# Kernel optimization log

Hardware: AMD Instinct MI355X
Metric: run time of the kernel (lower is better)

Reference implementation:

```python
import jax, jax.numpy as jnp
import numpy as np

N_NODES = 100000
N_EDGES = 1200000
D_IN = 64
D_HID = 64
D_OUT = 64


def setup_inputs() -> dict:
    key = jax.random.key(0)
    ks = jax.random.split(key, 9)
    x = jax.random.normal(ks[0], (N_NODES, D_IN), dtype=jnp.float32)
    edge_index = jax.random.randint(ks[1], (2, N_EDGES), 0, N_NODES, dtype=jnp.int32)
    edge_attr = jax.random.uniform(ks[2], (N_EDGES,), dtype=jnp.float32)
    def lin(k, fan_in, fan_out):
        s = 1.0 / np.sqrt(fan_in)
        return jax.random.uniform(k, (fan_in, fan_out), jnp.float32, -s, s)
    W1 = lin(ks[3], D_IN, D_HID)
    b1 = jnp.zeros((D_HID,), jnp.float32)
    W2 = lin(ks[4], D_HID, D_HID)
    b2 = jnp.zeros((D_HID,), jnp.float32)
    W3 = lin(ks[5], D_HID, D_OUT)
    b3 = jnp.zeros((D_OUT,), jnp.float32)
    return {"x": x, "edge_index": edge_index, "edge_attr": edge_attr,
            "W1": W1, "b1": b1, "W2": W2, "b2": b2, "W3": W3, "b3": b3}


def _gcn_norm(edge_index, edge_weight, num_nodes):
    # PyG GCNConv default: add self-loops (weight 1) then symmetric normalization
    src, dst = edge_index[0], edge_index[1]
    loop = jnp.arange(num_nodes, dtype=src.dtype)
    src_f = jnp.concatenate([src, loop])
    dst_f = jnp.concatenate([dst, loop])
    w_f = jnp.concatenate([edge_weight, jnp.ones((num_nodes,), edge_weight.dtype)])
    deg = jax.ops.segment_sum(w_f, dst_f, num_segments=num_nodes)
    dinv = jnp.where(deg > 0, jax.lax.rsqrt(jnp.maximum(deg, 1e-30)), 0.0)
    norm = dinv[src_f] * w_f * dinv[dst_f]  # [E + N]
    return src_f, dst_f, norm


def _gcn_layer(x, src, dst, norm, W, b, num_nodes):
    h = x @ W                                   # [N, d_out] (tiny GEMM)
    msg = h[src] * norm[:, None]                # gather + scale, [E+N, d_out]
    agg = jax.ops.segment_sum(msg, dst, num_segments=num_nodes)  # scatter-add
    return agg + b


def reference(x, edge_index, edge_attr, W1, b1, W2, b2, W3, b3):
    n = x.shape[0]
    src, dst, norm = _gcn_norm(edge_index, edge_attr, n)
    h = jax.nn.relu(_gcn_layer(x, src, dst, norm, W1, b1, n))
    h = jax.nn.relu(_gcn_layer(h, src, dst, norm, W2, b2, n))
    h = jax.nn.relu(_gcn_layer(h, src, dst, norm, W3, b3, n))
    return h
```

## Files before the change

### kernel.cpp

```cpp
#include <hip/hip_runtime.h>
#include <hip/hip_bf16.h>
#include <math.h>


#define MASK44 ((1ull << 44) - 1)

__global__ __launch_bounds__(256) void init_k(unsigned long long* packed, int N) {
    int i = blockIdx.x * blockDim.x + threadIdx.x;
    if (i < N) packed[i] = 0ull;
}

__global__ __launch_bounds__(256) void edge_pass_k(const int* __restrict__ dst,
                                                   const float* __restrict__ w,
                                                   unsigned long long* __restrict__ packed,
                                                   int* __restrict__ rank, int E) {
    int t = blockIdx.x * blockDim.x + threadIdx.x;
    int e = t * 8;
    if (e + 7 < E) {
        int4   da = *(const int4*)(dst + e);
        int4   db = *(const int4*)(dst + e + 4);
        float4 wa = *(const float4*)(w + e);
        float4 wb = *(const float4*)(w + e + 4);
        unsigned long long o0 = atomicAdd(&packed[da.x], (1ull << 44) + (unsigned long long)((double)wa.x * 4294967296.0));
        unsigned long long o1 = atomicAdd(&packed[da.y], (1ull << 44) + (unsigned long long)((double)wa.y * 4294967296.0));
        unsigned long long o2 = atomicAdd(&packed[da.z], (1ull << 44) + (unsigned long long)((double)wa.z * 4294967296.0));
        unsigned long long o3 = atomicAdd(&packed[da.w], (1ull << 44) + (unsigned long long)((double)wa.w * 4294967296.0));
        unsigned long long o4 = atomicAdd(&packed[db.x], (1ull << 44) + (unsigned long long)((double)wb.x * 4294967296.0));
        unsigned long long o5 = atomicAdd(&packed[db.y], (1ull << 44) + (unsigned long long)((double)wb.y * 4294967296.0));
        unsigned long long o6 = atomicAdd(&packed[db.z], (1ull << 44) + (unsigned long long)((double)wb.z * 4294967296.0));
        unsigned long long o7 = atomicAdd(&packed[db.w], (1ull << 44) + (unsigned long long)((double)wb.w * 4294967296.0));
        *(int4*)(rank + e)     = make_int4((int)(o0 >> 44), (int)(o1 >> 44),
                                           (int)(o2 >> 44), (int)(o3 >> 44));
        *(int4*)(rank + e + 4) = make_int4((int)(o4 >> 44), (int)(o5 >> 44),
                                           (int)(o6 >> 44), (int)(o7 >> 44));
    } else {
        for (int k = e; k < E; ++k) {
            unsigned long long o =
                atomicAdd(&packed[dst[k]], (1ull << 44) + (unsigned long long)((double)w[k] * 4294967296.0));
            rank[k] = (int)(o >> 44);
        }
    }
}

__global__ __launch_bounds__(1024) void scan_block_k(const unsigned long long* __restrict__ packed,
                                                     float* __restrict__ dinv,
                                                     int* __restrict__ tmp,
                                                     int* __restrict__ bsum, int N) {
    __shared__ int sm[1024];
    int tid = threadIdx.x;
    int g = blockIdx.x * 1024 + tid;
    unsigned long long pk = (g < N) ? packed[g] : 0ull;
    int v = (int)(pk >> 44);
    if (g < N) {
        double deg = 1.0 + (double)(pk & MASK44) * (1.0 / 4294967296.0);
        dinv[g] = (float)(1.0 / sqrt(deg));
    }
    sm[tid] = v;
    __syncthreads();
    for (int off = 1; off < 1024; off <<= 1) {
        int t = (tid >= off) ? sm[tid - off] : 0;
        __syncthreads();
        sm[tid] += t;
        __syncthreads();
    }
    if (g < N) tmp[g] = sm[tid] - v;
    if (tid == 1023) bsum[blockIdx.x] = sm[1023];
}

__global__ __launch_bounds__(1024) void scan_bsums_k(int* bsum, int nb, int* rowptr, int N) {
    __shared__ int sm[1024];
    int tid = threadIdx.x;
    int v = (tid < nb) ? bsum[tid] : 0;
    sm[tid] = v;
    __syncthreads();
    for (int off = 1; off < 1024; off <<= 1) {
        int t = (tid >= off) ? sm[tid - off] : 0;
        __syncthreads();
        sm[tid] += t;
        __syncthreads();
    }
    if (tid < nb) bsum[tid] = sm[tid] - v;
    if (tid == 1023) rowptr[N] = sm[1023];
}

__global__ __launch_bounds__(1024) void scan_add_k(const int* __restrict__ tmp,
                                                   const int* __restrict__ bsum,
                                                   int* __restrict__ rowptr, int N) {
    int g = blockIdx.x * 1024 + threadIdx.x;
    if (g < N) rowptr[g] = tmp[g] + bsum[blockIdx.x];
}

__global__ __launch_bounds__(256) void fill_csr_k(const int* __restrict__ src,
                                                  const int* __restrict__ dst,
                                                  const float* __restrict__ w,
                                                  const float* __restrict__ dinv,
                                                  const int* __restrict__ rowptr,
                                                  const int* __restrict__ rank,
                                                  int2* __restrict__ csr, int E) {
    int t = blockIdx.x * blockDim.x + threadIdx.x;
    int e = t * 8;
    if (e + 7 < E) {
        int4   sa = *(const int4*)(src + e);
        int4   sb = *(const int4*)(src + e + 4);
        int4   da = *(const int4*)(dst + e);
        int4   db = *(const int4*)(dst + e + 4);
        int4   ra = *(const int4*)(rank + e);
        int4   rb = *(const int4*)(rank + e + 4);
        float4 wa = *(const float4*)(w + e);
        float4 wb = *(const float4*)(w + e + 4);
        int p0 = rowptr[da.x] + ra.x;
        int p1 = rowptr[da.y] + ra.y;
        int p2 = rowptr[da.z] + ra.z;
        int p3 = rowptr[da.w] + ra.w;
        int p4 = rowptr[db.x] + rb.x;
        int p5 = rowptr[db.y] + rb.y;
        int p6 = rowptr[db.z] + rb.z;
        int p7 = rowptr[db.w] + rb.w;
        csr[p0] = make_int2(sa.x, __float_as_int(dinv[sa.x] * wa.x * dinv[da.x]));
        csr[p1] = make_int2(sa.y, __float_as_int(dinv[sa.y] * wa.y * dinv[da.y]));
        csr[p2] = make_int2(sa.z, __float_as_int(dinv[sa.z] * wa.z * dinv[da.z]));
        csr[p3] = make_int2(sa.w, __float_as_int(dinv[sa.w] * wa.w * dinv[da.w]));
        csr[p4] = make_int2(sb.x, __float_as_int(dinv[sb.x] * wb.x * dinv[db.x]));
        csr[p5] = make_int2(sb.y, __float_as_int(dinv[sb.y] * wb.y * dinv[db.y]));
        csr[p6] = make_int2(sb.z, __float_as_int(dinv[sb.z] * wb.z * dinv[db.z]));
        csr[p7] = make_int2(sb.w, __float_as_int(dinv[sb.w] * wb.w * dinv[db.w]));
    } else {
        for (int k = e; k < E; ++k) {
            int d = dst[k], s = src[k];
            int pos = rowptr[d] + rank[k];
            csr[pos] = make_int2(s, __float_as_int(dinv[s] * w[k] * dinv[d]));
        }
    }
}

__global__ __launch_bounds__(256) void gemm64_k(const float* __restrict__ X,
                                                const float* __restrict__ W,
                                                float* __restrict__ H, int N) {
    __shared__ float Wl[64 * 64];
    __shared__ float Xl[64 * 68];
    int tid = threadIdx.x;
    for (int i = tid; i < 4096; i += 256) Wl[i] = W[i];
    int row0 = blockIdx.x * 64;
    {
        int r = tid >> 6, c = tid & 63;
        #pragma unroll
        for (int p = 0; p < 16; ++p) {
            int rr = r + 4 * p;
            int grow = row0 + rr;
            Xl[rr * 68 + c] = (grow < N) ? X[(size_t)grow * 64 + c] : 0.0f;
        }
    }
    __syncthreads();
    int tc = tid & 15, tr = tid >> 4;
    float acc[4][4];
    #pragma unroll
    for (int i = 0; i < 4; ++i)
        #pragma unroll
        for (int j = 0; j < 4; ++j) acc[i][j] = 0.0f;

    #pragma unroll 8
    for (int k = 0; k < 64; ++k) {
        float4 wv = *(const float4*)&Wl[k * 64 + 4 * tc];
        float x0 = Xl[(4 * tr + 0) * 68 + k];
        float x1 = Xl[(4 * tr + 1) * 68 + k];
        float x2 = Xl[(4 * tr + 2) * 68 + k];
        float x3 = Xl[(4 * tr + 3) * 68 + k];
        acc[0][0] += x0 * wv.x; acc[0][1] += x0 * wv.y; acc[0][2] += x0 * wv.z; acc[0][3] += x0 * wv.w;
        acc[1][0] += x1 * wv.x; acc[1][1] += x1 * wv.y; acc[1][2] += x1 * wv.z; acc[1][3] += x1 * wv.w;
        acc[2][0] += x2 * wv.x; acc[2][1] += x2 * wv.y; acc[2][2] += x2 * wv.z; acc[2][3] += x2 * wv.w;
        acc[3][0] += x3 * wv.x; acc[3][1] += x3 * wv.y; acc[3][2] += x3 * wv.z; acc[3][3] += x3 * wv.w;
    }
    #pragma unroll
    for (int i = 0; i < 4; ++i) {
        int grow = row0 + 4 * tr + i;
        if (grow < N) {
            float4 st = make_float4(acc[i][0], acc[i][1], acc[i][2], acc[i][3]);
            *(float4*)&H[(size_t)grow * 64 + 4 * tc] = st;
        }
    }
}

__global__ __launch_bounds__(256) void agg_k(const float* __restrict__ H,
                                             const int* __restrict__ rowptr,
                                             const int2* __restrict__ csr,
                                             const float* __restrict__ dinv,
                                             const float* __restrict__ bias,
                                             float* __restrict__ out, int N) {
    int wave = (blockIdx.x * blockDim.x + threadIdx.x) >> 6;
    int lane = threadIdx.x & 63;
    if (wave >= N) return;
    int i = wave;
    int g = lane >> 4;
    int l = lane & 15;

    float di = dinv[i];
    float4 acc0, acc1;
    {
        float4 hv = *(const float4*)&H[(size_t)i * 64 + 4 * l];
        float s = (g == 0) ? (di * di) : 0.0f;
        acc0.x = hv.x * s; acc0.y = hv.y * s; acc0.z = hv.z * s; acc0.w = hv.w * s;
        acc1.x = 0.0f; acc1.y = 0.0f; acc1.z = 0.0f; acc1.w = 0.0f;
    }

    int e0 = rowptr[i], e1 = rowptr[i + 1];
    int e = e0;
    while (e < e1) {
        int nb = e1 - e;
        if (nb > 64) nb = 64;
        int2 m = (lane < nb) ? csr[e + lane] : make_int2(0, 0);
        #pragma unroll 4
        for (int j = 0; j < nb; j += 8) {
            int   sl0 = j + g;
            int   sj0 = __shfl(m.x, sl0);
            float nj0 = __shfl(__int_as_float(m.y), sl0);
            int   has1 = (j + 4 < nb);
            int   sl1 = has1 ? (j + 4 + g) : sl0;
            int   sj1 = __shfl(m.x, sl1);
            float nj1 = has1 ? __shfl(__int_as_float(m.y), sl1) : 0.0f;
            float4 hv0 = *(const float4*)&H[(size_t)sj0 * 64 + 4 * l];
            float4 hv1 = *(const float4*)&H[(size_t)sj1 * 64 + 4 * l];
            acc0.x += hv0.x * nj0; acc0.y += hv0.y * nj0;
            acc0.z += hv0.z * nj0; acc0.w += hv0.w * nj0;
            acc1.x += hv1.x * nj1; acc1.y += hv1.y * nj1;
            acc1.z += hv1.z * nj1; acc1.w += hv1.w * nj1;
        }
        e += nb;
    }

    float4 acc;
    acc.x = acc0.x + acc1.x; acc.y = acc0.y + acc1.y;
    acc.z = acc0.z + acc1.z; acc.w = acc0.w + acc1.w;

    acc.x += __shfl_xor(acc.x, 16); acc.y += __shfl_xor(acc.y, 16);
    acc.z += __shfl_xor(acc.z, 16); acc.w += __shfl_xor(acc.w, 16);
    acc.x += __shfl_xor(acc.x, 32); acc.y += __shfl_xor(acc.y, 32);
    acc.z += __shfl_xor(acc.z, 32); acc.w += __shfl_xor(acc.w, 32);

    if (g == 0) {
        float4 bv = *(const float4*)&bias[4 * l];
        float4 st;
        st.x = fmaxf(acc.x + bv.x, 0.0f);
        st.y = fmaxf(acc.y + bv.y, 0.0f);
        st.z = fmaxf(acc.z + bv.z, 0.0f);
        st.w = fmaxf(acc.w + bv.w, 0.0f);
        *(float4*)&out[(size_t)i * 64 + 4 * l] = st;
    }
}


extern "C" void kernel_launch(void* const* d_in, const int* in_sizes, int n_in,
                              void* d_out, int out_size, void* d_ws, size_t ws_size,
                              hipStream_t stream) {
    const float* x   = (const float*)d_in[0];
    const int*   ei  = (const int*)d_in[1];
    const float* ew  = (const float*)d_in[2];
    const float* W1  = (const float*)d_in[3];
    const float* b1  = (const float*)d_in[4];
    const float* W2  = (const float*)d_in[5];
    const float* b2  = (const float*)d_in[6];
    const float* W3  = (const float*)d_in[7];
    const float* b3  = (const float*)d_in[8];
    float* out = (float*)d_out;

    const int N = in_sizes[0] / 64;
    const int E = in_sizes[1] / 2;
    const int* src = ei;
    const int* dst = ei + E;

    char* p = (char*)d_ws;
    size_t off = 0;
    auto carve = [&](size_t bytes) -> void* {
        void* q = p + off;
        off += (bytes + 255) & ~(size_t)255;
        return q;
    };
    unsigned long long* packed = (unsigned long long*)carve((size_t)N * 8);
    float* dinv   = (float*)carve((size_t)N * 4);
    int*   tmp    = (int*)  carve((size_t)N * 4);
    int*   rowptr = (int*)  carve((size_t)(N + 1) * 4);
    int*   bsum   = (int*)  carve((size_t)1024 * 4);
    int*   rank   = (int*)  carve((size_t)E * 4);
    int2*  csr    = (int2*) carve((size_t)E * 8);
    float* Hbuf   = (float*)carve((size_t)N * 64 * 4);
    float* Abuf   = (float*)carve((size_t)N * 64 * 4);
    (void)ws_size;

    const int nB  = (N + 255) / 256;
    const int e8B = ((E + 7) / 8 + 255) / 256;
    const int nb  = (N + 1023) / 1024;
    const int gB  = (N + 63) / 64;
    const int aB  = (N * 64 + 255) / 256;

    init_k<<<nB, 256, 0, stream>>>(packed, N);
    edge_pass_k<<<e8B, 256, 0, stream>>>(dst, ew, packed, rank, E);
    scan_block_k<<<nb, 1024, 0, stream>>>(packed, dinv, tmp, bsum, N);
    scan_bsums_k<<<1, 1024, 0, stream>>>(bsum, nb, rowptr, N);
    scan_add_k<<<nb, 1024, 0, stream>>>(tmp, bsum, rowptr, N);
    fill_csr_k<<<e8B, 256, 0, stream>>>(src, dst, ew, dinv, rowptr, rank, csr, E);

    gemm64_k<<<gB, 256, 0, stream>>>(x, W1, Hbuf, N);
    agg_k<<<aB, 256, 0, stream>>>(Hbuf, rowptr, csr, dinv, b1, Abuf, N);
    gemm64_k<<<gB, 256, 0, stream>>>(Abuf, W2, Hbuf, N);
    agg_k<<<aB, 256, 0, stream>>>(Hbuf, rowptr, csr, dinv, b2, Abuf, N);
    gemm64_k<<<gB, 256, 0, stream>>>(Abuf, W3, Hbuf, N);
    agg_k<<<aB, 256, 0, stream>>>(Hbuf, rowptr, csr, dinv, b3, out, N);
}
```

Before: 415.3 us.

## Co-schedule first GEMM with edge-degree pass and fold block-sum scan into add

Merges the layer-1 GEMM and the atomic degree/rank edge pass into one launch, interleaving 8 GEMM blocks with 3 edge blocks per group of 11 so atomic-bound and compute-bound work share the GPU. It also removes the single-block bsum scan kernel by having every scan_add block redo the small 128-entry block-sum scan in shared memory. This cuts two launches and lets independent work overlap, at the cost of more shared memory per block in the fused kernel and a hard limit of 128 scan blocks.

```diff
diff --git a/kernel.cpp b/kernel.cpp
--- a/kernel.cpp
+++ b/kernel.cpp
@@ -10,34 +10,89 @@
     if (i < N) packed[i] = 0ull;
 }
 
-__global__ __launch_bounds__(256) void edge_pass_k(const int* __restrict__ dst,
-                                                   const float* __restrict__ w,
-                                                   unsigned long long* __restrict__ packed,
-                                                   int* __restrict__ rank, int E) {
-    int t = blockIdx.x * blockDim.x + threadIdx.x;
-    int e = t * 8;
-    if (e + 7 < E) {
-        int4   da = *(const int4*)(dst + e);
-        int4   db = *(const int4*)(dst + e + 4);
-        float4 wa = *(const float4*)(w + e);
-        float4 wb = *(const float4*)(w + e + 4);
-        unsigned long long o0 = atomicAdd(&packed[da.x], (1ull << 44) + (unsigned long long)((double)wa.x * 4294967296.0));
-        unsigned long long o1 = atomicAdd(&packed[da.y], (1ull << 44) + (unsigned long long)((double)wa.y * 4294967296.0));
-        unsigned long long o2 = atomicAdd(&packed[da.z], (1ull << 44) + (unsigned long long)((double)wa.z * 4294967296.0));
-        unsigned long long o3 = atomicAdd(&packed[da.w], (1ull << 44) + (unsigned long long)((double)wa.w * 4294967296.0));
-        unsigned long long o4 = atomicAdd(&packed[db.x], (1ull << 44) + (unsigned long long)((double)wb.x * 4294967296.0));
-        unsigned long long o5 = atomicAdd(&packed[db.y], (1ull << 44) + (unsigned long long)((double)wb.y * 4294967296.0));
-        unsigned long long o6 = atomicAdd(&packed[db.z], (1ull << 44) + (unsigned long long)((double)wb.z * 4294967296.0));
-        unsigned long long o7 = atomicAdd(&packed[db.w], (1ull << 44) + (unsigned long long)((double)wb.w * 4294967296.0));
-        *(int4*)(rank + e)     = make_int4((int)(o0 >> 44), (int)(o1 >> 44),
-                                           (int)(o2 >> 44), (int)(o3 >> 44));
-        *(int4*)(rank + e + 4) = make_int4((int)(o4 >> 44), (int)(o5 >> 44),
-                                           (int)(o6 >> 44), (int)(o7 >> 44));
+__global__ __launch_bounds__(256) void edge_gemm1_k(const int* __restrict__ dst,
+                                                    const float* __restrict__ w,
+                                                    unsigned long long* __restrict__ packed,
+                                                    int* __restrict__ rank, int E,
+                                                    const float* __restrict__ X,
+                                                    const float* __restrict__ W1,
+                                                    float* __restrict__ H, int N,
+                                                    int gB, int eB) {
+    __shared__ float Wl[64 * 64];
+    __shared__ float Xl[64 * 68];
+    int bid = blockIdx.x;
+    int q = bid / 11, r = bid % 11;
+    int tid = threadIdx.x;
+
+    if (r < 8) {
+        int gb = q * 8 + r;
+        if (gb >= gB) return;
+        for (int i = tid; i < 4096; i += 256) Wl[i] = W1[i];
+        int row0 = gb * 64;
+        {
+            int rr0 = tid >> 6, c = tid & 63;
+            #pragma unroll
+            for (int p = 0; p < 16; ++p) {
+                int rr = rr0 + 4 * p;
+                int grow = row0 + rr;
+                Xl[rr * 68 + c] = (grow < N) ? X[(size_t)grow * 64 + c] : 0.0f;
+            }
+        }
+        __syncthreads();
+        int tc = tid & 15, tr = tid >> 4;
+        float acc[4][4];
+        #pragma unroll
+        for (int i = 0; i < 4; ++i)
+            #pragma unroll
+            for (int j = 0; j < 4; ++j) acc[i][j] = 0.0f;
+        #pragma unroll 8
+        for (int k = 0; k < 64; ++k) {
+            float4 wv = *(const float4*)&Wl[k * 64 + 4 * tc];
+            float x0 = Xl[(4 * tr + 0) * 68 + k];
+            float x1 = Xl[(4 * tr + 1) * 68 + k];
+            float x2 = Xl[(4 * tr + 2) * 68 + k];
+            float x3 = Xl[(4 * tr + 3) * 68 + k];
+            acc[0][0] += x0 * wv.x; acc[0][1] += x0 * wv.y; acc[0][2] += x0 * wv.z; acc[0][3] += x0 * wv.w;
+            acc[1][0] += x1 * wv.x; acc[1][1] += x1 * wv.y; acc[1][2] += x1 * wv.z; acc[1][3] += x1 * wv.w;
+            acc[2][0] += x2 * wv.x; acc[2][1] += x2 * wv.y; acc[2][2] += x2 * wv.z; acc[2][3] += x2 * wv.w;
+            acc[3][0] += x3 * wv.x; acc[3][1] += x3 * wv.y; acc[3][2] += x3 * wv.z; acc[3][3] += x3 * wv.w;
+        }
+        #pragma unroll
+        for (int i = 0; i < 4; ++i) {
+            int grow = row0 + 4 * tr + i;
+            if (grow < N) {
+                float4 st = make_float4(acc[i][0], acc[i][1], acc[i][2], acc[i][3]);
+                *(float4*)&H[(size_t)grow * 64 + 4 * tc] = st;
+            }
+        }
     } else {
-        for (int k = e; k < E; ++k) {
-            unsigned long long o =
-                atomicAdd(&packed[dst[k]], (1ull << 44) + (unsigned long long)((double)w[k] * 4294967296.0));
-            rank[k] = (int)(o >> 44);
+        int eb = q * 3 + (r - 8);
+        if (eb >= eB) return;
+        int t = eb * 256 + tid;
+        int e = t * 8;
+        if (e + 7 < E) {
+            int4   da = *(const int4*)(dst + e);
+            int4   db = *(const int4*)(dst + e + 4);
+            float4 wa = *(const float4*)(w + e);
+            float4 wb = *(const float4*)(w + e + 4);
+            unsigned long long o0 = atomicAdd(&packed[da.x], (1ull << 44) + (unsigned long long)((double)wa.x * 4294967296.0));
+            unsigned long long o1 = atomicAdd(&packed[da.y], (1ull << 44) + (unsigned long long)((double)wa.y * 4294967296.0));
+            unsigned long long o2 = atomicAdd(&packed[da.z], (1ull << 44) + (unsigned long long)((double)wa.z * 4294967296.0));
+            unsigned long long o3 = atomicAdd(&packed[da.w], (1ull << 44) + (unsigned long long)((double)wa.w * 4294967296.0));
+            unsigned long long o4 = atomicAdd(&packed[db.x], (1ull << 44) + (unsigned long long)((double)wb.x * 4294967296.0));
+            unsigned long long o5 = atomicAdd(&packed[db.y], (1ull << 44) + (unsigned long long)((double)wb.y * 4294967296.0));
+            unsigned long long o6 = atomicAdd(&packed[db.z], (1ull << 44) + (unsigned long long)((double)wb.z * 4294967296.0));
+            unsigned long long o7 = atomicAdd(&packed[db.w], (1ull << 44) + (unsigned long long)((double)wb.w * 4294967296.0));
+            *(int4*)(rank + e)     = make_int4((int)(o0 >> 44), (int)(o1 >> 44),
+                                               (int)(o2 >> 44), (int)(o3 >> 44));
+            *(int4*)(rank + e + 4) = make_int4((int)(o4 >> 44), (int)(o5 >> 44),
+                                               (int)(o6 >> 44), (int)(o7 >> 44));
+        } else {
+            for (int k = e; k < E; ++k) {
+                unsigned long long o =
+                    atomicAdd(&packed[dst[k]], (1ull << 44) + (unsigned long long)((double)w[k] * 4294967296.0));
+                rank[k] = (int)(o >> 44);
+            }
         }
     }
 }
@@ -67,27 +122,24 @@
     if (tid == 1023) bsum[blockIdx.x] = sm[1023];
 }
 
-__global__ __launch_bounds__(1024) void scan_bsums_k(int* bsum, int nb, int* rowptr, int N) {
-    __shared__ int sm[1024];
-    int tid = threadIdx.x;
-    int v = (tid < nb) ? bsum[tid] : 0;
-    sm[tid] = v;
-    __syncthreads();
-    for (int off = 1; off < 1024; off <<= 1) {
-        int t = (tid >= off) ? sm[tid - off] : 0;
-        __syncthreads();
-        sm[tid] += t;
-        __syncthreads();
-    }
-    if (tid < nb) bsum[tid] = sm[tid] - v;
-    if (tid == 1023) rowptr[N] = sm[1023];
-}
-
 __global__ __launch_bounds__(1024) void scan_add_k(const int* __restrict__ tmp,
                                                    const int* __restrict__ bsum,
-                                                   int* __restrict__ rowptr, int N) {
-    int g = blockIdx.x * 1024 + threadIdx.x;
-    if (g < N) rowptr[g] = tmp[g] + bsum[blockIdx.x];
+                                                   int* __restrict__ rowptr, int N, int nb) {
+    __shared__ int sb[128];
+    int tid = threadIdx.x;
+    if (tid < 128) sb[tid] = (tid < nb) ? bsum[tid] : 0;
+    __syncthreads();
+    #pragma unroll
+    for (int off = 1; off < 128; off <<= 1) {
+        int v = (tid < 128 && tid >= off) ? sb[tid - off] : 0;
+        __syncthreads();
+        if (tid < 128) sb[tid] += v;
+        __syncthreads();
+    }
+    int prefix = (blockIdx.x > 0) ? sb[blockIdx.x - 1] : 0;
+    int g = blockIdx.x * 1024 + tid;
+    if (g < N) rowptr[g] = tmp[g] + prefix;
+    if (blockIdx.x == 0 && tid == 0) rowptr[N] = sb[nb - 1];
 }
 
 __global__ __launch_bounds__(256) void fill_csr_k(const int* __restrict__ src,
@@ -286,19 +338,20 @@
     (void)ws_size;
 
     const int nB  = (N + 255) / 256;
-    const int e8B = ((E + 7) / 8 + 255) / 256;
+    const int eB  = ((E + 7) / 8 + 255) / 256;
+    const int gB  = (N + 63) / 64;
     const int nb  = (N + 1023) / 1024;
-    const int gB  = (N + 63) / 64;
     const int aB  = (N * 64 + 255) / 256;
+    const int fuseGroups = ((gB + 7) / 8 > (eB + 2) / 3) ? (gB + 7) / 8 : (eB + 2) / 3;
+    const int fB  = fuseGroups * 11;
 
     init_k<<<nB, 256, 0, stream>>>(packed, N);
-    edge_pass_k<<<e8B, 256, 0, stream>>>(dst, ew, packed, rank, E);
+    edge_gemm1_k<<<fB, 256, 0, stream>>>(dst, ew, packed, rank, E,
+                                         x, W1, Hbuf, N, gB, eB);
     scan_block_k<<<nb, 1024, 0, stream>>>(packed, dinv, tmp, bsum, N);
-    scan_bsums_k<<<1, 1024, 0, stream>>>(bsum, nb, rowptr, N);
-    scan_add_k<<<nb, 1024, 0, stream>>>(tmp, bsum, rowptr, N);
-    fill_csr_k<<<e8B, 256, 0, stream>>>(src, dst, ew, dinv, rowptr, rank, csr, E);
-
-    gemm64_k<<<gB, 256, 0, stream>>>(x, W1, Hbuf, N);
+    scan_add_k<<<nb, 1024, 0, stream>>>(tmp, bsum, rowptr, N, nb);
+    fill_csr_k<<<eB, 256, 0, stream>>>(src, dst, ew, dinv, rowptr, rank, csr, E);
+
     agg_k<<<aB, 256, 0, stream>>>(Hbuf, rowptr, csr, dinv, b1, Abuf, N);
     gemm64_k<<<gB, 256, 0, stream>>>(Abuf, W2, Hbuf, N);
     agg_k<<<aB, 256, 0, stream>>>(Hbuf, rowptr, csr, dinv, b2, Abuf, N);
```

After: 400.5 us. -3.6%, faster.
